# Optimization experiments

Measured on AMD Instinct MI355X. Metric: run time of the kernel, lower is better.

Reference implementation:

```python
import jax, jax.numpy as jnp
import numpy as np

N_NODES = 100000
N_EDGES = 1600000
D_IN = 128
D_HID = 128
N_CLASS = 10
N_GRAPHS = 512
BN_EPS = 1e-5


def setup_inputs() -> dict:
    key = jax.random.key(0)
    ks = jax.random.split(key, 12)
    x = jax.random.normal(ks[0], (N_NODES, D_IN), dtype=jnp.float32)
    edge_index = jax.random.randint(ks[1], (2, N_EDGES), 0, N_NODES, dtype=jnp.int32)
    idx = jnp.sort(jax.random.randint(ks[2], (N_NODES,), 0, N_GRAPHS, dtype=jnp.int32))
    s = 1.0 / np.sqrt(D_HID)
    W1 = jax.random.uniform(ks[3], (D_IN, D_HID), minval=-s, maxval=s, dtype=jnp.float32)
    b1 = jnp.zeros((D_HID,), jnp.float32)
    W2 = jax.random.uniform(ks[4], (D_HID, D_HID), minval=-s, maxval=s, dtype=jnp.float32)
    b2 = jnp.zeros((D_HID,), jnp.float32)
    W3 = jax.random.uniform(ks[5], (D_HID, D_HID), minval=-s, maxval=s, dtype=jnp.float32)
    b3 = jnp.zeros((D_HID,), jnp.float32)
    W4 = jax.random.uniform(ks[6], (D_HID, N_CLASS), minval=-s, maxval=s, dtype=jnp.float32)
    b4 = jnp.zeros((N_CLASS,), jnp.float32)
    gamma = jnp.ones((D_HID,), jnp.float32)
    beta = jnp.zeros((D_HID,), jnp.float32)
    return {"x": x, "edge_index": edge_index, "idx": idx,
            "W1": W1, "b1": b1, "W2": W2, "b2": b2,
            "W3": W3, "b3": b3, "W4": W4, "b4": b4,
            "gamma": gamma, "beta": beta}


def _agg(h, src, dst):
    # (adj + I) @ h : sum of neighbor features plus self-loop
    return jax.ops.segment_sum(h[src], dst, num_segments=N_NODES) + h


def reference(x, edge_index, idx, W1, b1, W2, b2, W3, b3, W4, b4, gamma, beta):
    src, dst = edge_index[0], edge_index[1]
    z1 = jax.nn.relu(_agg(x, src, dst) @ W1 + b1)          # [N, H] (dropout = identity, eval)
    h = _agg(z1, src, dst) @ W2 + b2                        # [N, H]
    pooled = jax.ops.segment_sum(h, idx, num_segments=N_GRAPHS)  # [G, H] scatter-add readout
    # BatchNorm1d over graph (batch) dimension, training-mode batch stats
    mean = jnp.mean(pooled, axis=0)
    var = jnp.var(pooled, axis=0)
    out = (pooled - mean) * jax.lax.rsqrt(var + BN_EPS) * gamma + beta
    zg = jax.nn.relu(out @ W3 + b3)
    logits = zg @ W4 + b4                                   # [G, C]
    return jax.nn.log_softmax(logits, axis=1)
```

## Files before the change

kernel.cpp:

```cpp
#include <hip/hip_runtime.h>
#include <hip/hip_fp16.h>
#include <math.h>

#define NN 100000
#define NE 1600000
#define DH 128
#define NG 512
#define NC 10
#define NSEG 8
#define SEGN 12500
#define CHE 8192
#define NCH 196
#define MAXDEG 48

#define NB_HIST (NCH * NSEG)
#define NB_CNT  98
#define NB_GEMM ((NN + 63) / 64)


typedef __attribute__((ext_vector_type(8))) _Float16 f16x8;
typedef __attribute__((ext_vector_type(4))) float f32x4;
typedef __attribute__((ext_vector_type(4))) int i32x4;


__global__ __launch_bounds__(256, 4) void k_build(
    const int* __restrict__ dst, const int* __restrict__ src,
    int* __restrict__ counts, int* __restrict__ csr,
    const int* __restrict__ gidx, int* __restrict__ cnt,
    const float* __restrict__ A, const float* __restrict__ W,
    __half* __restrict__ out) {
    int b = blockIdx.x;
    int t = threadIdx.x;
    if (b < NB_HIST) {
        int seg = b & 7;
        int chunk = b >> 3;
        int lo = seg * SEGN, hi = lo + SEGN;
        int e0 = chunk * CHE;
        int e1 = e0 + CHE < NE ? e0 + CHE : NE;
        for (int e = e0 + t * 4; e < e1; e += 1024) {
            i32x4 d4 = __builtin_nontemporal_load((const i32x4*)(dst + e));
            bool i0 = d4.x >= lo && d4.x < hi;
            bool i1 = d4.y >= lo && d4.y < hi;
            bool i2 = d4.z >= lo && d4.z < hi;
            bool i3 = d4.w >= lo && d4.w < hi;
            i32x4 s4 = {0, 0, 0, 0};
            if (i0 | i1 | i2 | i3)
                s4 = __builtin_nontemporal_load((const i32x4*)(src + e));
            if (i0) {
                int p = atomicAdd(&counts[d4.x], 1);
                if (p < MAXDEG) csr[d4.x * MAXDEG + p] = s4.x;
            }
            if (i1) {
                int p = atomicAdd(&counts[d4.y], 1);
                if (p < MAXDEG) csr[d4.y * MAXDEG + p] = s4.y;
            }
            if (i2) {
                int p = atomicAdd(&counts[d4.z], 1);
                if (p < MAXDEG) csr[d4.z * MAXDEG + p] = s4.z;
            }
            if (i3) {
                int p = atomicAdd(&counts[d4.w], 1);
                if (p < MAXDEG) csr[d4.w * MAXDEG + p] = s4.w;
            }
        }
    } else if (b < NB_HIST + NB_CNT) {
        int cb = b - NB_HIST;
        int n0 = cb * 1024 + t * 4;
        if (n0 >= NN) return;
        int g = gidx[n0];
        int run = 1;
        for (int j = 1; j < 4; ++j) {
            int n = n0 + j;
            if (n < NN) {
                int gg = gidx[n];
                if (gg == g) {
                    run++;
                } else {
                    atomicAdd(&cnt[g], run);
                    g = gg;
                    run = 1;
                }
            }
        }
        atomicAdd(&cnt[g], run);
    } else {
        __shared__ _Float16 sWT[DH * 128];
        int gb = b - (NB_HIST + NB_CNT);
        int wv = t >> 6;
        int lane = t & 63;
        for (int i = t; i < DH * DH; i += 256) {
            int k = i >> 7, n = i & 127;
            sWT[n * 128 + (((k >> 3) ^ (n & 15)) * 8) + (k & 7)] = (_Float16)W[i];
        }
        __syncthreads();

        int m = lane & 15;
        int quad = lane >> 4;
        int node0 = gb * 64 + wv * 16;
        int nodeA = node0 + m;
        if (nodeA >= NN) nodeA = NN - 1;
        const float* arow = A + (size_t)nodeA * DH;

        f16x8 afrag[4];
#pragma unroll
        for (int kt = 0; kt < 4; ++kt) {
            int k0 = kt * 32 + quad * 8;
            f32x4 u0 = __builtin_nontemporal_load((const f32x4*)(arow + k0));
            f32x4 u1 = __builtin_nontemporal_load((const f32x4*)(arow + k0 + 4));
            afrag[kt][0] = (_Float16)u0.x; afrag[kt][1] = (_Float16)u0.y;
            afrag[kt][2] = (_Float16)u0.z; afrag[kt][3] = (_Float16)u0.w;
            afrag[kt][4] = (_Float16)u1.x; afrag[kt][5] = (_Float16)u1.y;
            afrag[kt][6] = (_Float16)u1.z; afrag[kt][7] = (_Float16)u1.w;
        }

        f32x4 acc0 = {0.f, 0.f, 0.f, 0.f};
        f32x4 acc1 = acc0, acc2 = acc0, acc3 = acc0;
        f32x4 acc4 = acc0, acc5 = acc0, acc6 = acc0, acc7 = acc0;
#pragma unroll
        for (int kt = 0; kt < 4; ++kt) {
            int kb = kt * 4 + quad;
            const _Float16* wbase = &sWT[(size_t)m * 128 + ((kb ^ m) * 8)];
            acc0 = __builtin_amdgcn_mfma_f32_16x16x32_f16(afrag[kt], *(const f16x8*)(wbase + 0 * 16 * 128), acc0, 0, 0, 0);
            acc1 = __builtin_amdgcn_mfma_f32_16x16x32_f16(afrag[kt], *(const f16x8*)(wbase + 1 * 16 * 128), acc1, 0, 0, 0);
            acc2 = __builtin_amdgcn_mfma_f32_16x16x32_f16(afrag[kt], *(const f16x8*)(wbase + 2 * 16 * 128), acc2, 0, 0, 0);
            acc3 = __builtin_amdgcn_mfma_f32_16x16x32_f16(afrag[kt], *(const f16x8*)(wbase + 3 * 16 * 128), acc3, 0, 0, 0);
            acc4 = __builtin_amdgcn_mfma_f32_16x16x32_f16(afrag[kt], *(const f16x8*)(wbase + 4 * 16 * 128), acc4, 0, 0, 0);
            acc5 = __builtin_amdgcn_mfma_f32_16x16x32_f16(afrag[kt], *(const f16x8*)(wbase + 5 * 16 * 128), acc5, 0, 0, 0);
            acc6 = __builtin_amdgcn_mfma_f32_16x16x32_f16(afrag[kt], *(const f16x8*)(wbase + 6 * 16 * 128), acc6, 0, 0, 0);
            acc7 = __builtin_amdgcn_mfma_f32_16x16x32_f16(afrag[kt], *(const f16x8*)(wbase + 7 * 16 * 128), acc7, 0, 0, 0);
        }

#pragma unroll
        for (int r = 0; r < 4; ++r) {
            int node = node0 + quad * 4 + r;
            if (node < NN) {
                uint4 o;
                *(__half2*)&o.x = __floats2half2_rn(acc0[r], acc1[r]);
                *(__half2*)&o.y = __floats2half2_rn(acc2[r], acc3[r]);
                *(__half2*)&o.z = __floats2half2_rn(acc4[r], acc5[r]);
                *(__half2*)&o.w = __floats2half2_rn(acc6[r], acc7[r]);
                ((uint4*)out)[(size_t)node * 16 + m] = o;
            }
        }
    }
}


__device__ __forceinline__ void acc8(float* a, const uint4& v, float m) {
    float2 f;
    f = __half22float2(*(const __half2*)&v.x); a[0] = fmaf(m, f.x, a[0]); a[1] = fmaf(m, f.y, a[1]);
    f = __half22float2(*(const __half2*)&v.y); a[2] = fmaf(m, f.x, a[2]); a[3] = fmaf(m, f.y, a[3]);
    f = __half22float2(*(const __half2*)&v.z); a[4] = fmaf(m, f.x, a[4]); a[5] = fmaf(m, f.y, a[5]);
    f = __half22float2(*(const __half2*)&v.w); a[6] = fmaf(m, f.x, a[6]); a[7] = fmaf(m, f.y, a[7]);
}


__global__ __launch_bounds__(256, 4) void k_agg_h(
    const __half* __restrict__ in, const int* __restrict__ counts,
    const int* __restrict__ csr, const float* __restrict__ bias,
    __half* __restrict__ outA) {
    int t = threadIdx.x;
    int lane = t & 15;
    int node = blockIdx.x * 16 + (t >> 4);
    const uint4* in4 = (const uint4*)in;
    float a[8];
#pragma unroll
    for (int j = 0; j < 8; ++j) a[j] = 0.f;
    uint4 sv = in4[(size_t)node * 16 + lane];
    acc8(a, sv, 1.f);
    int e0 = node * MAXDEG;
    int deg = counts[node];
    deg = deg < MAXDEG ? deg : MAXDEG;
    int e1 = e0 + deg;
    int elast = e1 - 1;
    for (int e = e0; e < e1; e += 8) {
        int idx[8];
        float m[8];
#pragma unroll
        for (int i = 0; i < 8; ++i) {
            int ei = e + i;
            int ec = ei < elast ? ei : elast;
            idx[i] = csr[ec];
            m[i] = (ei < e1) ? 1.f : 0.f;
        }
        uint4 v[8];
#pragma unroll
        for (int i = 0; i < 8; ++i) v[i] = in4[(size_t)idx[i] * 16 + lane];
#pragma unroll
        for (int i = 0; i < 8; ++i) acc8(a, v[i], m[i]);
    }
    float bj[8];
#pragma unroll
    for (int j = 0; j < 8; ++j) bj[j] = bias[j * 16 + lane];
#pragma unroll
    for (int j = 0; j < 8; ++j) a[j] = fmaxf(a[j] + bj[j], 0.f);
    uint4 o;
    *(__half2*)&o.x = __floats2half2_rn(a[0], a[1]);
    *(__half2*)&o.y = __floats2half2_rn(a[2], a[3]);
    *(__half2*)&o.z = __floats2half2_rn(a[4], a[5]);
    *(__half2*)&o.w = __floats2half2_rn(a[6], a[7]);
    ((uint4*)outA)[(size_t)node * 16 + lane] = o;
}


__global__ __launch_bounds__(256, 4) void k_agg_pool_h(
    const __half* __restrict__ in, const int* __restrict__ counts,
    const int* __restrict__ csr, const int* __restrict__ gidx,
    float* __restrict__ pp8) {
    __shared__ __align__(16) float sA[16][DH];
    int t = threadIdx.x;
    int lane = t & 15;
    int p = t >> 4;
    int node0 = blockIdx.x * 16;
    int node = node0 + p;
    const uint4* in4 = (const uint4*)in;
    float a[8];
#pragma unroll
    for (int j = 0; j < 8; ++j) a[j] = 0.f;
    uint4 sv = in4[(size_t)node * 16 + lane];
    acc8(a, sv, 1.f);
    int e0 = node * MAXDEG;
    int deg = counts[node];
    deg = deg < MAXDEG ? deg : MAXDEG;
    int e1 = e0 + deg;
    int elast = e1 - 1;
    for (int e = e0; e < e1; e += 8) {
        int idx[8];
        float m[8];
#pragma unroll
        for (int i = 0; i < 8; ++i) {
            int ei = e + i;
            int ec = ei < elast ? ei : elast;
            idx[i] = csr[ec];
            m[i] = (ei < e1) ? 1.f : 0.f;
        }
        uint4 v[8];
#pragma unroll
        for (int i = 0; i < 8; ++i) v[i] = in4[(size_t)idx[i] * 16 + lane];
#pragma unroll
        for (int i = 0; i < 8; ++i) acc8(a, v[i], m[i]);
    }
    float4* row = (float4*)&sA[p][lane * 8];
    row[0] = make_float4(a[0], a[1], a[2], a[3]);
    row[1] = make_float4(a[4], a[5], a[6], a[7]);
    __syncthreads();
    if (t < DH) {
        float* pp = pp8 + (size_t)(blockIdx.x & 7) * NG * DH;
        int gprev = gidx[node0];
        float run = 0.f;
        for (int q = 0; q < 16; ++q) {
            int g = gidx[node0 + q];
            if (g != gprev) {
                atomicAdd(&pp[gprev * DH + t], run);
                run = 0.f;
                gprev = g;
            }
            run += sA[q][t];
        }
        atomicAdd(&pp[gprev * DH + t], run);
    }
}


__device__ __forceinline__ void fma4(float4& acc, float s, const float4& wv) {
    acc.x = fmaf(s, wv.x, acc.x);
    acc.y = fmaf(s, wv.y, acc.y);
    acc.z = fmaf(s, wv.z, acc.z);
    acc.w = fmaf(s, wv.w, acc.w);
}


__global__ __launch_bounds__(256, 2) void k_pool_mm(
    const float* __restrict__ pp8, const float* __restrict__ W,
    const float* __restrict__ bias, const int* __restrict__ cnt,
    float* __restrict__ pooled) {
    __shared__ __align__(16) float sW[DH * DH];
    __shared__ __align__(16) float sA[32 * DH];
    int t = threadIdx.x;
    int g0 = blockIdx.x * 32;
    {
        const float4* W4g = (const float4*)W;
        float4* sW4 = (float4*)sW;
        for (int i = t; i < DH * DH / 4; i += 256) {
            int r = i >> 5;
            int orig = ((r & 7) << 4) + (r >> 3);
            sW4[i] = W4g[orig * 32 + (i & 31)];
        }
        const float4* P4 = (const float4*)pp8;
        float4* sA4 = (float4*)sA;
        for (int i = t; i < 32 * DH / 4; i += 256) {
            float4 s;
            s.x = 0.f; s.y = 0.f; s.z = 0.f; s.w = 0.f;
#pragma unroll
            for (int c = 0; c < NSEG; ++c) {
                float4 v = P4[(size_t)c * NG * DH / 4 + (size_t)g0 * DH / 4 + i];
                s.x += v.x; s.y += v.y; s.z += v.z; s.w += v.w;
            }
            sA4[i] = s;
        }
    }
    __syncthreads();

    int c4 = t & 31;
    int n0 = (t >> 5) * 4;
    const float4* sA4 = (const float4*)sA;
    const float4* sW4 = (const float4*)sW;
    float4 acc0, acc1, acc2, acc3;
    acc0.x = acc0.y = acc0.z = acc0.w = 0.f;
    acc1 = acc0; acc2 = acc0; acc3 = acc0;

#pragma unroll 2
    for (int kc = 0; kc < DH / 4; ++kc) {
        float4 a0 = sA4[(n0 + 0) * 32 + kc];
        float4 a1 = sA4[(n0 + 1) * 32 + kc];
        float4 a2 = sA4[(n0 + 2) * 32 + kc];
        float4 a3 = sA4[(n0 + 3) * 32 + kc];
        float4 w0 = sW4[(4 * kc + 0) * 32 + c4];
        float4 w1 = sW4[(4 * kc + 1) * 32 + c4];
        float4 w2 = sW4[(4 * kc + 2) * 32 + c4];
        float4 w3 = sW4[(4 * kc + 3) * 32 + c4];
        fma4(acc0, a0.x, w0); fma4(acc0, a0.y, w1); fma4(acc0, a0.z, w2); fma4(acc0, a0.w, w3);
        fma4(acc1, a1.x, w0); fma4(acc1, a1.y, w1); fma4(acc1, a1.z, w2); fma4(acc1, a1.w, w3);
        fma4(acc2, a2.x, w0); fma4(acc2, a2.y, w1); fma4(acc2, a2.z, w2); fma4(acc2, a2.w, w3);
        fma4(acc3, a3.x, w0); fma4(acc3, a3.y, w1); fma4(acc3, a3.z, w2); fma4(acc3, a3.w, w3);
    }

    float4 b2v = ((const float4*)bias)[c4];
    float c0 = (float)cnt[g0 + n0 + 0];
    float c1 = (float)cnt[g0 + n0 + 1];
    float c2 = (float)cnt[g0 + n0 + 2];
    float c3 = (float)cnt[g0 + n0 + 3];
    fma4(acc0, c0, b2v);
    fma4(acc1, c1, b2v);
    fma4(acc2, c2, b2v);
    fma4(acc3, c3, b2v);

    float4* out4 = (float4*)pooled;
    out4[(size_t)(g0 + n0 + 0) * 32 + c4] = acc0;
    out4[(size_t)(g0 + n0 + 1) * 32 + c4] = acc1;
    out4[(size_t)(g0 + n0 + 2) * 32 + c4] = acc2;
    out4[(size_t)(g0 + n0 + 3) * 32 + c4] = acc3;
}


__global__ void k_bnstats(const float* __restrict__ pooled, float* __restrict__ mean,
                          float* __restrict__ rstd) {
    int c = blockIdx.x;
    int l = threadIdx.x;
    float s = 0.f, s2 = 0.f;
    for (int g = l; g < NG; g += 64) {
        float v = pooled[g * DH + c];
        s += v;
        s2 += v * v;
    }
#pragma unroll
    for (int off = 32; off > 0; off >>= 1) {
        s += __shfl_down(s, off, 64);
        s2 += __shfl_down(s2, off, 64);
    }
    if (l == 0) {
        float m = s * (1.f / NG);
        float var = s2 * (1.f / NG) - m * m;
        mean[c] = m;
        rstd[c] = rsqrtf(var + 1e-5f);
    }
}


__global__ __launch_bounds__(128) void k_tail(
    const float* __restrict__ pooled, const float* __restrict__ mean,
    const float* __restrict__ rstd, const float* __restrict__ gamma,
    const float* __restrict__ beta, const float* __restrict__ W3,
    const float* __restrict__ b3, const float* __restrict__ W4,
    const float* __restrict__ b4, float* __restrict__ out) {
    __shared__ __align__(16) float sW[DH * DH];
    __shared__ float sg[DH];
    __shared__ float sz[DH];
    __shared__ float slog[NC];
    __shared__ float slse;
    int g = blockIdx.x, t = threadIdx.x;
    {
        const float4* W34 = (const float4*)W3;
        float4* sW4 = (float4*)sW;
        for (int i = t; i < DH * DH / 4; i += 128) sW4[i] = W34[i];
    }
    float v = pooled[g * DH + t];
    v = (v - mean[t]) * rstd[t] * gamma[t] + beta[t];
    sg[t] = v;
    __syncthreads();
    float acc = b3[t];
#pragma unroll 4
    for (int k = 0; k < DH; ++k) acc = fmaf(sg[k], sW[k * DH + t], acc);
    sz[t] = fmaxf(acc, 0.f);
    __syncthreads();
    if (t < NC) {
        float a = b4[t];
        for (int k = 0; k < DH; ++k) a = fmaf(sz[k], W4[k * NC + t], a);
        slog[t] = a;
    }
    __syncthreads();
    if (t == 0) {
        float mx = slog[0];
        for (int j = 1; j < NC; ++j) mx = fmaxf(mx, slog[j]);
        float se = 0.f;
        for (int j = 0; j < NC; ++j) se += expf(slog[j] - mx);
        slse = mx + logf(se);
    }
    __syncthreads();
    if (t < NC) out[g * NC + t] = slog[t] - slse;
}


extern "C" void kernel_launch(void* const* d_in, const int* in_sizes, int n_in,
                              void* d_out, int out_size, void* d_ws, size_t ws_size,
                              hipStream_t stream) {
    const float* x = (const float*)d_in[0];
    const int* ei = (const int*)d_in[1];
    const int* src = ei;
    const int* dst = ei + NE;
    const int* gidx = (const int*)d_in[2];
    const float* W1 = (const float*)d_in[3];
    const float* b1 = (const float*)d_in[4];
    const float* W2 = (const float*)d_in[5];
    const float* b2 = (const float*)d_in[6];
    const float* W3 = (const float*)d_in[7];
    const float* b3 = (const float*)d_in[8];
    const float* W4 = (const float*)d_in[9];
    const float* b4 = (const float*)d_in[10];
    const float* gamma = (const float*)d_in[11];
    const float* beta = (const float*)d_in[12];
    float* out = (float*)d_out;

    char* w = (char*)d_ws;
    auto take = [&](size_t bytes) {
        char* p = w;
        w += (bytes + 255) & ~size_t(255);
        return p;
    };
    int* counts = (int*)take((size_t)NN * 4);
    int* cnt = (int*)take((size_t)NG * 4);
    float* pp8 = (float*)take((size_t)NSEG * NG * DH * 4);
    size_t zero_bytes = (size_t)((char*)(pp8 + (size_t)NSEG * NG * DH) - (char*)counts);
    int* csr = (int*)take((size_t)NN * MAXDEG * 4);
    __half* y = (__half*)take((size_t)NN * DH * 2);
    __half* z1 = (__half*)take((size_t)NN * DH * 2);
    float* pooled = (float*)take((size_t)NG * DH * 4);
    float* meanb = (float*)take(DH * 4);
    float* rstdb = (float*)take(DH * 4);

    hipMemsetAsync(counts, 0, zero_bytes, stream);

    k_build<<<NB_HIST + NB_CNT + NB_GEMM, 256, 0, stream>>>(
        dst, src, counts, csr, gidx, cnt, x, W1, y);

    k_agg_h<<<NN / 16, 256, 0, stream>>>(y, counts, csr, b1, z1);

    k_agg_pool_h<<<NN / 16, 256, 0, stream>>>(z1, counts, csr, gidx, pp8);
    k_pool_mm<<<NG / 32, 256, 0, stream>>>(pp8, W2, b2, cnt, pooled);

    k_bnstats<<<DH, 64, 0, stream>>>(pooled, meanb, rstdb);
    k_tail<<<NG, 128, 0, stream>>>(pooled, meanb, rstdb, gamma, beta, W3, b3, W4, b4, out);
}
```

Before: 358.5 us.

## Split fused build kernel into separate histogram and GEMM kernels

Splits the combined CSR-build/graph-count/GEMM kernel into two launches: a histogram kernel with higher occupancy bounds (256,8) and no shared memory, and a standalone MFMA GEMM kernel. The histogram loop now processes 8 edges per thread and always loads src, instead of loading it only when some destination falls in the segment. The aim is to stop the GEMM's 32KB shared memory and register demand from limiting occupancy of the atomic-heavy histogram blocks. In exchange it adds a launch and serializes the two phases that could previously overlap within one grid.

```diff
diff --git a/kernel.cpp b/kernel.cpp
--- a/kernel.cpp
+++ b/kernel.cpp
@@ -23,12 +23,19 @@
 typedef __attribute__((ext_vector_type(4))) int i32x4;
 
 
-__global__ __launch_bounds__(256, 4) void k_build(
+__device__ __forceinline__ void upd_edge(int d, int s, int lo, int hi,
+                                         int* __restrict__ counts,
+                                         int* __restrict__ csr) {
+    if (d >= lo && d < hi) {
+        int p = atomicAdd(&counts[d], 1);
+        if (p < MAXDEG) csr[d * MAXDEG + p] = s;
+    }
+}
+
+__global__ __launch_bounds__(256, 8) void k_hist(
     const int* __restrict__ dst, const int* __restrict__ src,
     int* __restrict__ counts, int* __restrict__ csr,
-    const int* __restrict__ gidx, int* __restrict__ cnt,
-    const float* __restrict__ A, const float* __restrict__ W,
-    __half* __restrict__ out) {
+    const int* __restrict__ gidx, int* __restrict__ cnt) {
     int b = blockIdx.x;
     int t = threadIdx.x;
     if (b < NB_HIST) {
@@ -37,33 +44,21 @@
         int lo = seg * SEGN, hi = lo + SEGN;
         int e0 = chunk * CHE;
         int e1 = e0 + CHE < NE ? e0 + CHE : NE;
-        for (int e = e0 + t * 4; e < e1; e += 1024) {
-            i32x4 d4 = __builtin_nontemporal_load((const i32x4*)(dst + e));
-            bool i0 = d4.x >= lo && d4.x < hi;
-            bool i1 = d4.y >= lo && d4.y < hi;
-            bool i2 = d4.z >= lo && d4.z < hi;
-            bool i3 = d4.w >= lo && d4.w < hi;
-            i32x4 s4 = {0, 0, 0, 0};
-            if (i0 | i1 | i2 | i3)
-                s4 = __builtin_nontemporal_load((const i32x4*)(src + e));
-            if (i0) {
-                int p = atomicAdd(&counts[d4.x], 1);
-                if (p < MAXDEG) csr[d4.x * MAXDEG + p] = s4.x;
-            }
-            if (i1) {
-                int p = atomicAdd(&counts[d4.y], 1);
-                if (p < MAXDEG) csr[d4.y * MAXDEG + p] = s4.y;
-            }
-            if (i2) {
-                int p = atomicAdd(&counts[d4.z], 1);
-                if (p < MAXDEG) csr[d4.z * MAXDEG + p] = s4.z;
-            }
-            if (i3) {
-                int p = atomicAdd(&counts[d4.w], 1);
-                if (p < MAXDEG) csr[d4.w * MAXDEG + p] = s4.w;
-            }
-        }
-    } else if (b < NB_HIST + NB_CNT) {
+        for (int e = e0 + t * 8; e < e1; e += 2048) {
+            i32x4 da = __builtin_nontemporal_load((const i32x4*)(dst + e));
+            i32x4 db = __builtin_nontemporal_load((const i32x4*)(dst + e + 4));
+            i32x4 sa = __builtin_nontemporal_load((const i32x4*)(src + e));
+            i32x4 sb = __builtin_nontemporal_load((const i32x4*)(src + e + 4));
+            upd_edge(da.x, sa.x, lo, hi, counts, csr);
+            upd_edge(da.y, sa.y, lo, hi, counts, csr);
+            upd_edge(da.z, sa.z, lo, hi, counts, csr);
+            upd_edge(da.w, sa.w, lo, hi, counts, csr);
+            upd_edge(db.x, sb.x, lo, hi, counts, csr);
+            upd_edge(db.y, sb.y, lo, hi, counts, csr);
+            upd_edge(db.z, sb.z, lo, hi, counts, csr);
+            upd_edge(db.w, sb.w, lo, hi, counts, csr);
+        }
+    } else {
         int cb = b - NB_HIST;
         int n0 = cb * 1024 + t * 4;
         if (n0 >= NN) return;
@@ -83,64 +78,70 @@
             }
         }
         atomicAdd(&cnt[g], run);
-    } else {
-        __shared__ _Float16 sWT[DH * 128];
-        int gb = b - (NB_HIST + NB_CNT);
-        int wv = t >> 6;
-        int lane = t & 63;
-        for (int i = t; i < DH * DH; i += 256) {
-            int k = i >> 7, n = i & 127;
-            sWT[n * 128 + (((k >> 3) ^ (n & 15)) * 8) + (k & 7)] = (_Float16)W[i];
-        }
-        __syncthreads();
-
-        int m = lane & 15;
-        int quad = lane >> 4;
-        int node0 = gb * 64 + wv * 16;
-        int nodeA = node0 + m;
-        if (nodeA >= NN) nodeA = NN - 1;
-        const float* arow = A + (size_t)nodeA * DH;
-
-        f16x8 afrag[4];
-#pragma unroll
-        for (int kt = 0; kt < 4; ++kt) {
-            int k0 = kt * 32 + quad * 8;
-            f32x4 u0 = __builtin_nontemporal_load((const f32x4*)(arow + k0));
-            f32x4 u1 = __builtin_nontemporal_load((const f32x4*)(arow + k0 + 4));
-            afrag[kt][0] = (_Float16)u0.x; afrag[kt][1] = (_Float16)u0.y;
-            afrag[kt][2] = (_Float16)u0.z; afrag[kt][3] = (_Float16)u0.w;
-            afrag[kt][4] = (_Float16)u1.x; afrag[kt][5] = (_Float16)u1.y;
-            afrag[kt][6] = (_Float16)u1.z; afrag[kt][7] = (_Float16)u1.w;
-        }
-
-        f32x4 acc0 = {0.f, 0.f, 0.f, 0.f};
-        f32x4 acc1 = acc0, acc2 = acc0, acc3 = acc0;
-        f32x4 acc4 = acc0, acc5 = acc0, acc6 = acc0, acc7 = acc0;
-#pragma unroll
-        for (int kt = 0; kt < 4; ++kt) {
-            int kb = kt * 4 + quad;
-            const _Float16* wbase = &sWT[(size_t)m * 128 + ((kb ^ m) * 8)];
-            acc0 = __builtin_amdgcn_mfma_f32_16x16x32_f16(afrag[kt], *(const f16x8*)(wbase + 0 * 16 * 128), acc0, 0, 0, 0);
-            acc1 = __builtin_amdgcn_mfma_f32_16x16x32_f16(afrag[kt], *(const f16x8*)(wbase + 1 * 16 * 128), acc1, 0, 0, 0);
-            acc2 = __builtin_amdgcn_mfma_f32_16x16x32_f16(afrag[kt], *(const f16x8*)(wbase + 2 * 16 * 128), acc2, 0, 0, 0);
-            acc3 = __builtin_amdgcn_mfma_f32_16x16x32_f16(afrag[kt], *(const f16x8*)(wbase + 3 * 16 * 128), acc3, 0, 0, 0);
-            acc4 = __builtin_amdgcn_mfma_f32_16x16x32_f16(afrag[kt], *(const f16x8*)(wbase + 4 * 16 * 128), acc4, 0, 0, 0);
-            acc5 = __builtin_amdgcn_mfma_f32_16x16x32_f16(afrag[kt], *(const f16x8*)(wbase + 5 * 16 * 128), acc5, 0, 0, 0);
-            acc6 = __builtin_amdgcn_mfma_f32_16x16x32_f16(afrag[kt], *(const f16x8*)(wbase + 6 * 16 * 128), acc6, 0, 0, 0);
-            acc7 = __builtin_amdgcn_mfma_f32_16x16x32_f16(afrag[kt], *(const f16x8*)(wbase + 7 * 16 * 128), acc7, 0, 0, 0);
-        }
-
-#pragma unroll
-        for (int r = 0; r < 4; ++r) {
-            int node = node0 + quad * 4 + r;
-            if (node < NN) {
-                uint4 o;
-                *(__half2*)&o.x = __floats2half2_rn(acc0[r], acc1[r]);
-                *(__half2*)&o.y = __floats2half2_rn(acc2[r], acc3[r]);
-                *(__half2*)&o.z = __floats2half2_rn(acc4[r], acc5[r]);
-                *(__half2*)&o.w = __floats2half2_rn(acc6[r], acc7[r]);
-                ((uint4*)out)[(size_t)node * 16 + m] = o;
-            }
+    }
+}
+
+
+__global__ __launch_bounds__(256, 4) void k_gemm(
+    const float* __restrict__ A, const float* __restrict__ W,
+    __half* __restrict__ out) {
+    __shared__ _Float16 sWT[DH * 128];
+    int gb = blockIdx.x;
+    int t = threadIdx.x;
+    int wv = t >> 6;
+    int lane = t & 63;
+    for (int i = t; i < DH * DH; i += 256) {
+        int k = i >> 7, n = i & 127;
+        sWT[n * 128 + (((k >> 3) ^ (n & 15)) * 8) + (k & 7)] = (_Float16)W[i];
+    }
+    __syncthreads();
+
+    int m = lane & 15;
+    int quad = lane >> 4;
+    int node0 = gb * 64 + wv * 16;
+    int nodeA = node0 + m;
+    if (nodeA >= NN) nodeA = NN - 1;
+    const float* arow = A + (size_t)nodeA * DH;
+
+    f16x8 afrag[4];
+#pragma unroll
+    for (int kt = 0; kt < 4; ++kt) {
+        int k0 = kt * 32 + quad * 8;
+        f32x4 u0 = __builtin_nontemporal_load((const f32x4*)(arow + k0));
+        f32x4 u1 = __builtin_nontemporal_load((const f32x4*)(arow + k0 + 4));
+        afrag[kt][0] = (_Float16)u0.x; afrag[kt][1] = (_Float16)u0.y;
+        afrag[kt][2] = (_Float16)u0.z; afrag[kt][3] = (_Float16)u0.w;
+        afrag[kt][4] = (_Float16)u1.x; afrag[kt][5] = (_Float16)u1.y;
+        afrag[kt][6] = (_Float16)u1.z; afrag[kt][7] = (_Float16)u1.w;
+    }
+
+    f32x4 acc0 = {0.f, 0.f, 0.f, 0.f};
+    f32x4 acc1 = acc0, acc2 = acc0, acc3 = acc0;
+    f32x4 acc4 = acc0, acc5 = acc0, acc6 = acc0, acc7 = acc0;
+#pragma unroll
+    for (int kt = 0; kt < 4; ++kt) {
+        int kb = kt * 4 + quad;
+        const _Float16* wbase = &sWT[(size_t)m * 128 + ((kb ^ m) * 8)];
+        acc0 = __builtin_amdgcn_mfma_f32_16x16x32_f16(afrag[kt], *(const f16x8*)(wbase + 0 * 16 * 128), acc0, 0, 0, 0);
+        acc1 = __builtin_amdgcn_mfma_f32_16x16x32_f16(afrag[kt], *(const f16x8*)(wbase + 1 * 16 * 128), acc1, 0, 0, 0);
+        acc2 = __builtin_amdgcn_mfma_f32_16x16x32_f16(afrag[kt], *(const f16x8*)(wbase + 2 * 16 * 128), acc2, 0, 0, 0);
+        acc3 = __builtin_amdgcn_mfma_f32_16x16x32_f16(afrag[kt], *(const f16x8*)(wbase + 3 * 16 * 128), acc3, 0, 0, 0);
+        acc4 = __builtin_amdgcn_mfma_f32_16x16x32_f16(afrag[kt], *(const f16x8*)(wbase + 4 * 16 * 128), acc4, 0, 0, 0);
+        acc5 = __builtin_amdgcn_mfma_f32_16x16x32_f16(afrag[kt], *(const f16x8*)(wbase + 5 * 16 * 128), acc5, 0, 0, 0);
+        acc6 = __builtin_amdgcn_mfma_f32_16x16x32_f16(afrag[kt], *(const f16x8*)(wbase + 6 * 16 * 128), acc6, 0, 0, 0);
+        acc7 = __builtin_amdgcn_mfma_f32_16x16x32_f16(afrag[kt], *(const f16x8*)(wbase + 7 * 16 * 128), acc7, 0, 0, 0);
+    }
+
+#pragma unroll
+    for (int r = 0; r < 4; ++r) {
+        int node = node0 + quad * 4 + r;
+        if (node < NN) {
+            uint4 o;
+            *(__half2*)&o.x = __floats2half2_rn(acc0[r], acc1[r]);
+            *(__half2*)&o.y = __floats2half2_rn(acc2[r], acc3[r]);
+            *(__half2*)&o.z = __floats2half2_rn(acc4[r], acc5[r]);
+            *(__half2*)&o.w = __floats2half2_rn(acc6[r], acc7[r]);
+            ((uint4*)out)[(size_t)node * 16 + m] = o;
         }
     }
 }
@@ -450,8 +451,8 @@
 
     hipMemsetAsync(counts, 0, zero_bytes, stream);
 
-    k_build<<<NB_HIST + NB_CNT + NB_GEMM, 256, 0, stream>>>(
-        dst, src, counts, csr, gidx, cnt, x, W1, y);
+    k_hist<<<NB_HIST + NB_CNT, 256, 0, stream>>>(dst, src, counts, csr, gidx, cnt);
+    k_gemm<<<NB_GEMM, 256, 0, stream>>>(x, W1, y);
 
     k_agg_h<<<NN / 16, 256, 0, stream>>>(y, counts, csr, b1, z1);
 
```

After: 375.7 us. 4.8% more time.
